# Performance work log

Measured on AMD Instinct MI355X. Metric: run time of the kernel, lower is better.

The kernel has to match this reference:

```python
import jax, jax.numpy as jnp
import numpy as np

D_MODEL = 1024
NUM_HEADS = 16
HEAD_DIM = D_MODEL // NUM_HEADS


def setup_inputs() -> dict:
    key = jax.random.key(0)
    ks = jax.random.split(key, 5)
    x = jax.random.normal(ks[0], (2, 2048, D_MODEL), dtype=jnp.float32)
    # torch nn.Linear init scale ~ U(-1/sqrt(in), 1/sqrt(in)); use small normals
    s = 1.0 / np.sqrt(D_MODEL)
    W_qkv = jax.random.normal(ks[1], (D_MODEL, 3 * D_MODEL), dtype=jnp.float32) * s
    b_qkv = jax.random.normal(ks[2], (3 * D_MODEL,), dtype=jnp.float32) * s
    W_out = jax.random.normal(ks[3], (D_MODEL, D_MODEL), dtype=jnp.float32) * s
    b_out = jax.random.normal(ks[4], (D_MODEL,), dtype=jnp.float32) * s
    return {"x": x, "W_qkv": W_qkv, "b_qkv": b_qkv, "W_out": W_out, "b_out": b_out}


def reference(x, W_qkv, b_qkv, W_out, b_out):
    B, S, _ = x.shape
    qkv = x @ W_qkv + b_qkv                                  # [B,S,3D]
    qkv = qkv.reshape(B, S, NUM_HEADS, 3 * HEAD_DIM).transpose(0, 2, 1, 3)  # [B,H,S,3d]
    q, k, v = jnp.split(qkv, 3, axis=-1)                     # each [B,H,S,d]
    scale = 1.0 / np.sqrt(HEAD_DIM)
    scores = jnp.einsum("bhqd,bhkd->bhqk", q, k) * scale      # [B,H,S,S]
    attn = jax.nn.softmax(scores, axis=-1)
    values = jnp.einsum("bhqk,bhkd->bhqd", attn, v)           # [B,H,S,d]
    values = values.transpose(0, 2, 1, 3).reshape(B, S, D_MODEL)
    return values @ W_out + b_out
```

## Files before the change

kernel.cpp:

```cpp
#include <hip/hip_runtime.h>


#define D_MODEL 1024
#define NHEAD   16
#define HDIM    64
#define SEQ     2048
#define BATCH   2
#define NTOK    (BATCH * SEQ)

typedef float    f32x4  __attribute__((ext_vector_type(4)));
typedef float    f32x16 __attribute__((ext_vector_type(16)));
typedef _Float16 f16x8  __attribute__((ext_vector_type(8)));
typedef _Float16 f16x4  __attribute__((ext_vector_type(4)));

#define GLOBAL_LOAD_LDS16(gptr, lptr)                                            \
    __builtin_amdgcn_global_load_lds(                                            \
        (const __attribute__((address_space(1))) unsigned int*)(gptr),           \
        (__attribute__((address_space(3))) unsigned int*)(lptr), 16, 0, 0)

__global__ __launch_bounds__(256) void prep_kernel(
    const float* __restrict__ x, _Float16* __restrict__ xh,
    const float* __restrict__ Wqkv, _Float16* __restrict__ wq_t,
    const float* __restrict__ Wout, _Float16* __restrict__ wo_t)
{
    const int bx = blockIdx.x;
    const int tid = threadIdx.x;
    if (bx < 4096) {
        const int i = (bx * 256 + tid) * 4;
        const float4 v = *(const float4*)&x[i];
        f16x4 hh;
        hh[0] = (_Float16)v.x; hh[1] = (_Float16)v.y;
        hh[2] = (_Float16)v.z; hh[3] = (_Float16)v.w;
        *(f16x4*)&xh[i] = hh;
        return;
    }
    __shared__ float ts[64][65];
    const float* W; _Float16* Wt; int N, n0, k0;
    if (bx < 4096 + 768) {
        const int local = bx - 4096;
        W = Wqkv; Wt = wq_t; N = 3072;
        n0 = (local % 48) * 64; k0 = (local / 48) * 64;
    } else {
        const int local = bx - 4864;
        W = Wout; Wt = wo_t; N = 1024;
        n0 = (local % 16) * 64; k0 = (local / 16) * 64;
    }
    {
        const int r = tid >> 2, c = (tid & 3) << 4;
        const float* src = W + (size_t)(k0 + r) * N + n0 + c;
        #pragma unroll
        for (int u = 0; u < 4; ++u)
            *(float4*)&ts[r][c + u * 4] = *(const float4*)&src[u * 4];
    }
    __syncthreads();
    {
        const int n = tid >> 2, kg = (tid & 3) << 4;
        f16x8 v0, v1;
        #pragma unroll
        for (int j = 0; j < 8; ++j) {
            v0[j] = (_Float16)ts[kg + j][n];
            v1[j] = (_Float16)ts[kg + 8 + j][n];
        }
        _Float16* dst = Wt + (size_t)(n0 + n) * D_MODEL + k0 + kg;
        *(f16x8*)&dst[0] = v0;
        *(f16x8*)&dst[8] = v1;
    }
}

__global__ __launch_bounds__(512) void gemm_qkv_kernel(
    const _Float16* __restrict__ A, const _Float16* __restrict__ Bt,
    const float* __restrict__ bias, _Float16* __restrict__ Cout,
    int M, int N, int K)
{
    __shared__ _Float16 lds[2][4096];
    const int tid = threadIdx.x;
    const int wave = tid >> 6, lane = tid & 63;
    const int quad = lane >> 4, l16 = lane & 15;
    const int m0 = blockIdx.y * 128, n0 = blockIdx.x * 128;
    const int wr = wave >> 1, wc = wave & 1;

    f32x4 acc[2][4] = {};

    const bool isA = wave < 4;
    const _Float16* gsrc = isA ? (A + (size_t)m0 * K) : (Bt + (size_t)n0 * K);
    _Float16* ldst = isA ? &lds[0][0] : &lds[1][0];
    const int sbase = (wave & 3) * 2;

    for (int k0 = 0; k0 < K; k0 += 32) {
        __syncthreads();
        #pragma unroll
        for (int j = 0; j < 2; ++j) {
            const int seg = sbase + j;
            const int chunk = seg >> 1;
            const int row = ((seg & 1) << 6) | lane;
            GLOBAL_LOAD_LDS16(gsrc + (size_t)row * K + k0 + chunk * 8, ldst + seg * 512);
        }
        __syncthreads();

        f16x8 a[2], b[4];
        #pragma unroll
        for (int mt = 0; mt < 2; ++mt)
            a[mt] = *(const f16x8*)&lds[0][quad * 1024 + (wr * 32 + mt * 16 + l16) * 8];
        #pragma unroll
        for (int nt = 0; nt < 4; ++nt)
            b[nt] = *(const f16x8*)&lds[1][quad * 1024 + (wc * 64 + nt * 16 + l16) * 8];
        #pragma unroll
        for (int mt = 0; mt < 2; ++mt)
            #pragma unroll
            for (int nt = 0; nt < 4; ++nt)
                acc[mt][nt] = __builtin_amdgcn_mfma_f32_16x16x32_f16(a[mt], b[nt], acc[mt][nt], 0, 0, 0);
    }

    #pragma unroll
    for (int nt = 0; nt < 4; ++nt) {
        const int col = n0 + wc * 64 + nt * 16 + l16;
        const float bv = bias[col];
        #pragma unroll
        for (int mt = 0; mt < 2; ++mt) {
            #pragma unroll
            for (int r = 0; r < 4; ++r) {
                const int row = m0 + wr * 32 + mt * 16 + quad * 4 + r;
                Cout[(size_t)row * N + col] = (_Float16)(acc[mt][nt][r] + bv);
            }
        }
    }
}

__global__ __launch_bounds__(512) void gemm_out_kernel(
    const _Float16* __restrict__ A, const _Float16* __restrict__ Bt,
    const float* __restrict__ bias, float* __restrict__ Cout)
{
    const int K = D_MODEL, N = D_MODEL;
    __shared__ _Float16 ldsA[4096];
    __shared__ _Float16 ldsB[2048];
    const int tid = threadIdx.x;
    const int wave = tid >> 6, lane = tid & 63;
    const int quad = lane >> 4, l16 = lane & 15;
    const int m0 = blockIdx.y * 128, n0 = blockIdx.x * 64;
    const int wr = wave >> 1, wc = wave & 1;

    f32x4 acc[2][2] = {};

    for (int k0 = 0; k0 < K; k0 += 32) {
        __syncthreads();
        if (wave < 4) {
            #pragma unroll
            for (int j = 0; j < 2; ++j) {
                const int seg = wave * 2 + j;
                const int chunk = seg >> 1;
                const int row = ((seg & 1) << 6) | lane;
                GLOBAL_LOAD_LDS16(A + (size_t)(m0 + row) * K + k0 + chunk * 8, ldsA + seg * 512);
            }
        } else {
            const int seg = wave - 4;
            GLOBAL_LOAD_LDS16(Bt + (size_t)(n0 + lane) * K + k0 + seg * 8, ldsB + seg * 512);
        }
        __syncthreads();

        f16x8 a[2], b[2];
        #pragma unroll
        for (int mt = 0; mt < 2; ++mt)
            a[mt] = *(const f16x8*)&ldsA[quad * 1024 + (wr * 32 + mt * 16 + l16) * 8];
        #pragma unroll
        for (int nt = 0; nt < 2; ++nt)
            b[nt] = *(const f16x8*)&ldsB[quad * 512 + (wc * 32 + nt * 16 + l16) * 8];
        #pragma unroll
        for (int mt = 0; mt < 2; ++mt)
            #pragma unroll
            for (int nt = 0; nt < 2; ++nt)
                acc[mt][nt] = __builtin_amdgcn_mfma_f32_16x16x32_f16(a[mt], b[nt], acc[mt][nt], 0, 0, 0);
    }

    #pragma unroll
    for (int nt = 0; nt < 2; ++nt) {
        const int col = n0 + wc * 32 + nt * 16 + l16;
        const float bv = bias[col];
        #pragma unroll
        for (int mt = 0; mt < 2; ++mt) {
            #pragma unroll
            for (int r = 0; r < 4; ++r) {
                const int row = m0 + wr * 32 + mt * 16 + quad * 4 + r;
                Cout[(size_t)row * N + col] = acc[mt][nt][r] + bv;
            }
        }
    }
}

__global__ __launch_bounds__(256) void swizzle_kv_kernel(
    const _Float16* __restrict__ qkv,
    _Float16* __restrict__ Ksw, _Float16* __restrict__ Vsw)
{
    __shared__ _Float16 ts[64][72];
    const int tid = threadIdx.x;
    const int s0 = blockIdx.x * 64, h = blockIdx.y, b = blockIdx.z;
    const size_t hsz = (size_t)8 * SEQ * 8;
    _Float16* kh = Ksw + (size_t)(b * NHEAD + h) * hsz;
    _Float16* vh = Vsw + (size_t)(b * NHEAD + h) * hsz;

    {
        const int s = s0 + (tid >> 2);
        const int dg = (tid & 3) << 4;
        const _Float16* src = qkv + (size_t)(b * SEQ + s) * (3 * D_MODEL) + h * (3 * HDIM) + HDIM + dg;
        const f16x8 v0 = *(const f16x8*)&src[0];
        const f16x8 v1 = *(const f16x8*)&src[8];
        const int c0 = dg >> 3;
        *(f16x8*)&kh[((size_t)c0 * SEQ + s) * 8]       = v0;
        *(f16x8*)&kh[((size_t)(c0 + 1) * SEQ + s) * 8] = v1;
    }
    {
        const int s = tid >> 2, dg = (tid & 3) << 4;
        const _Float16* src = qkv + (size_t)(b * SEQ + s0 + s) * (3 * D_MODEL) + h * (3 * HDIM) + 2 * HDIM + dg;
        *(f16x8*)&ts[s][dg]     = *(const f16x8*)&src[0];
        *(f16x8*)&ts[s][dg + 8] = *(const f16x8*)&src[8];
    }
    __syncthreads();
    {
        const int d = tid >> 2, sg = (tid & 3) << 4;
        f16x8 v0, v1;
        #pragma unroll
        for (int j = 0; j < 8; ++j) { v0[j] = ts[sg + j][d]; v1[j] = ts[sg + 8 + j][d]; }
        const int cs0 = (s0 + sg) >> 3;
        *(f16x8*)&vh[((size_t)cs0 * HDIM + d) * 8]       = v0;
        *(f16x8*)&vh[((size_t)(cs0 + 1) * HDIM + d) * 8] = v1;
    }
}

__global__ __launch_bounds__(256) void attn_mfma_kernel(
    const _Float16* __restrict__ qkv,
    const _Float16* __restrict__ Ksw, const _Float16* __restrict__ Vsw,
    _Float16* __restrict__ val)
{
    __shared__ _Float16 Ks[2][4096];
    __shared__ _Float16 Vts[2][4096];

    const int tid = threadIdx.x;
    const int wave = tid >> 6, lane = tid & 63;
    const int l31 = lane & 31, hi = lane >> 5;

    const int id = blockIdx.x;
    const int g  = (id & 7) * 64 + (id >> 3);
    const int qt = g & 15, hb = g >> 4;
    const int h  = hb & 15, b = hb >> 4;
    const int q0 = qt * 128;

    const size_t hsz = (size_t)8 * SEQ * 8;
    const _Float16* kh = Ksw + (size_t)(b * NHEAD + h) * hsz;
    const _Float16* vh = Vsw + (size_t)(b * NHEAD + h) * hsz;

    f16x8 qf[4];
    {
        const int row = q0 + wave * 32 + l31;
        const _Float16* src = qkv + (size_t)(b * SEQ + row) * (3 * D_MODEL) + h * (3 * HDIM) + hi * 8;
        #pragma unroll
        for (int kk = 0; kk < 4; ++kk) {
            const f16x8 t = *(const f16x8*)(src + kk * 16);
            #pragma unroll
            for (int j = 0; j < 8; ++j)
                qf[kk][j] = (_Float16)((float)t[j] * 0.1803368802f);
        }
    }

    f32x16 acc0 = {};
    f32x16 acc1 = {};
    float rs = 0.f;

    #pragma unroll
    for (int jj = 0; jj < 2; ++jj) {
        const int c = wave * 2 + jj;
        GLOBAL_LOAD_LDS16(kh + ((size_t)c * SEQ + lane) * 8, &Ks[0][c * 512]);
        GLOBAL_LOAD_LDS16(vh + ((size_t)c * HDIM + lane) * 8, &Vts[0][c * 512]);
    }
    __syncthreads();

    for (int kt = 0; kt < SEQ / 64; ++kt) {
        const int cur = kt & 1;

        if (kt + 1 < SEQ / 64) {
            #pragma unroll
            for (int jj = 0; jj < 2; ++jj) {
                const int c = wave * 2 + jj;
                GLOBAL_LOAD_LDS16(kh + ((size_t)c * SEQ + (kt + 1) * 64 + lane) * 8,
                                  &Ks[cur ^ 1][c * 512]);
                GLOBAL_LOAD_LDS16(vh + ((size_t)((kt + 1) * 8 + c) * HDIM + lane) * 8,
                                  &Vts[cur ^ 1][c * 512]);
            }
        }

        f32x16 s0 = {};
        f32x16 s1 = {};
        __builtin_amdgcn_s_setprio(1);
        #pragma unroll
        for (int kk = 0; kk < 4; ++kk) {
            const f16x8 k0 = *(const f16x8*)&Ks[cur][(kk * 2 + hi) * 512 + l31 * 8];
            const f16x8 k1 = *(const f16x8*)&Ks[cur][(kk * 2 + hi) * 512 + (32 + l31) * 8];
            s0 = __builtin_amdgcn_mfma_f32_32x32x16_f16(k0, qf[kk], s0, 0, 0, 0);
            s1 = __builtin_amdgcn_mfma_f32_32x32x16_f16(k1, qf[kk], s1, 0, 0, 0);
        }
        __builtin_amdgcn_s_setprio(0);

        f16x8 pa[4];
        #pragma unroll
        for (int half = 0; half < 2; ++half) {
            const f32x16 sv = half ? s1 : s0;
            float p[16];
            #pragma unroll
            for (int r = 0; r < 16; ++r)
                p[r] = __builtin_amdgcn_exp2f(sv[r]);
            #pragma unroll
            for (int r = 0; r < 16; r += 4)
                rs += (p[r] + p[r + 1]) + (p[r + 2] + p[r + 3]);

            union { f16x8 h; unsigned u[4]; } lo, hh;
            {
                const unsigned A = __builtin_bit_cast(unsigned, __builtin_amdgcn_cvt_pkrtz(p[0], p[1]));
                const unsigned B = __builtin_bit_cast(unsigned, __builtin_amdgcn_cvt_pkrtz(p[2], p[3]));
                const unsigned C = __builtin_bit_cast(unsigned, __builtin_amdgcn_cvt_pkrtz(p[4], p[5]));
                const unsigned D = __builtin_bit_cast(unsigned, __builtin_amdgcn_cvt_pkrtz(p[6], p[7]));
                const auto rac = __builtin_amdgcn_permlane32_swap(A, C, false, false);
                const auto rbd = __builtin_amdgcn_permlane32_swap(B, D, false, false);
                lo.u[0] = rac[0]; lo.u[1] = rbd[0]; lo.u[2] = rac[1]; lo.u[3] = rbd[1];
            }
            {
                const unsigned E = __builtin_bit_cast(unsigned, __builtin_amdgcn_cvt_pkrtz(p[8],  p[9]));
                const unsigned F = __builtin_bit_cast(unsigned, __builtin_amdgcn_cvt_pkrtz(p[10], p[11]));
                const unsigned G = __builtin_bit_cast(unsigned, __builtin_amdgcn_cvt_pkrtz(p[12], p[13]));
                const unsigned H = __builtin_bit_cast(unsigned, __builtin_amdgcn_cvt_pkrtz(p[14], p[15]));
                const auto reg = __builtin_amdgcn_permlane32_swap(E, G, false, false);
                const auto rfh = __builtin_amdgcn_permlane32_swap(F, H, false, false);
                hh.u[0] = reg[0]; hh.u[1] = rfh[0]; hh.u[2] = reg[1]; hh.u[3] = rfh[1];
            }
            pa[half * 2]     = lo.h;
            pa[half * 2 + 1] = hh.h;
        }

        __builtin_amdgcn_s_setprio(1);
        #pragma unroll
        for (int ks = 0; ks < 4; ++ks) {
            const f16x8 v0 = *(const f16x8*)&Vts[cur][(ks * 2 + hi) * 512 + l31 * 8];
            const f16x8 v1 = *(const f16x8*)&Vts[cur][(ks * 2 + hi) * 512 + (32 + l31) * 8];
            acc0 = __builtin_amdgcn_mfma_f32_32x32x16_f16(pa[ks], v0, acc0, 0, 0, 0);
            acc1 = __builtin_amdgcn_mfma_f32_32x32x16_f16(pa[ks], v1, acc1, 0, 0, 0);
        }
        __builtin_amdgcn_s_setprio(0);

        __syncthreads();
    }

    rs += __shfl_xor(rs, 32);
    const float inv = 1.f / rs;

    #pragma unroll
    for (int r = 0; r < 16; ++r) {
        const int qo = (r & 3) + 8 * (r >> 2) + 4 * hi;
        const float invr = __shfl(inv, qo);
        const int row = b * SEQ + q0 + wave * 32 + qo;
        val[(size_t)row * D_MODEL + h * HDIM + l31]      = (_Float16)(acc0[r] * invr);
        val[(size_t)row * D_MODEL + h * HDIM + 32 + l31] = (_Float16)(acc1[r] * invr);
    }
}

extern "C" void kernel_launch(void* const* d_in, const int* in_sizes, int n_in,
                              void* d_out, int out_size, void* d_ws, size_t ws_size,
                              hipStream_t stream)
{
    const float* x     = (const float*)d_in[0];
    const float* W_qkv = (const float*)d_in[1];
    const float* b_qkv = (const float*)d_in[2];
    const float* W_out = (const float*)d_in[3];
    const float* b_out = (const float*)d_in[4];

    char* ws = (char*)d_ws;
    _Float16* Ksw   = (_Float16*)ws;
    _Float16* val_h = (_Float16*)(ws + (8u << 20));
    _Float16* wq_t  = (_Float16*)(ws + (16u << 20));
    _Float16* wo_t  = (_Float16*)(ws + (22u << 20));
    _Float16* qkv_h = (_Float16*)(ws + (24u << 20));
    _Float16* x_h   = (_Float16*)(ws + (48u << 20));
    _Float16* Vsw   = (_Float16*)(ws + (48u << 20));

    prep_kernel<<<5120, 256, 0, stream>>>(x, x_h, W_qkv, wq_t, W_out, wo_t);
    gemm_qkv_kernel<<<dim3(3 * D_MODEL / 128, NTOK / 128), 512, 0, stream>>>(
        x_h, wq_t, b_qkv, qkv_h, NTOK, 3 * D_MODEL, D_MODEL);
    swizzle_kv_kernel<<<dim3(SEQ / 64, NHEAD, BATCH), 256, 0, stream>>>(qkv_h, Ksw, Vsw);
    attn_mfma_kernel<<<dim3(512, 1, 1), 256, 0, stream>>>(qkv_h, Ksw, Vsw, val_h);
    gemm_out_kernel<<<dim3(D_MODEL / 64, NTOK / 128), 512, 0, stream>>>(
        val_h, wo_t, b_out, (float*)d_out);
}
```

Measured before the change: 223.7 us.

## Process two 32-row query tiles per wave to reuse K/V fragments and interleave softmax

Each wave now handles 64 query rows (two 32-row sub-tiles), so a block covers 256 queries and the grid halves to 256 blocks. K and V fragments are loaded from LDS into registers once per iteration and shared by both sub-tiles, halving LDS reads and global K/V traffic per query. The QK MFMAs of the second sub-tile are issued before the first sub-tile's softmax so that exp work can overlap matrix ops, and the explicit setprio hints are dropped. The cost is much higher register pressure and only 256 blocks, which may underfill the 256 CUs and reduce latency hiding.

Measured after the change: 228.4 us. 1.02x slower.

```diff
diff --git a/kernel.cpp b/kernel.cpp
--- a/kernel.cpp
+++ b/kernel.cpp
@@ -225,6 +225,44 @@
     }
 }
 
+__device__ __forceinline__ void softmax_frag(
+    const f32x16 s0, const f32x16 s1, float& rs, f16x8 pa[4])
+{
+    #pragma unroll
+    for (int half = 0; half < 2; ++half) {
+        const f32x16 sv = half ? s1 : s0;
+        float p[16];
+        #pragma unroll
+        for (int r = 0; r < 16; ++r)
+            p[r] = __builtin_amdgcn_exp2f(sv[r]);
+        #pragma unroll
+        for (int r = 0; r < 16; r += 4)
+            rs += (p[r] + p[r + 1]) + (p[r + 2] + p[r + 3]);
+
+        union { f16x8 hv; unsigned u[4]; } lo, hh;
+        {
+            const unsigned A = __builtin_bit_cast(unsigned, __builtin_amdgcn_cvt_pkrtz(p[0], p[1]));
+            const unsigned B = __builtin_bit_cast(unsigned, __builtin_amdgcn_cvt_pkrtz(p[2], p[3]));
+            const unsigned C = __builtin_bit_cast(unsigned, __builtin_amdgcn_cvt_pkrtz(p[4], p[5]));
+            const unsigned D = __builtin_bit_cast(unsigned, __builtin_amdgcn_cvt_pkrtz(p[6], p[7]));
+            const auto rac = __builtin_amdgcn_permlane32_swap(A, C, false, false);
+            const auto rbd = __builtin_amdgcn_permlane32_swap(B, D, false, false);
+            lo.u[0] = rac[0]; lo.u[1] = rbd[0]; lo.u[2] = rac[1]; lo.u[3] = rbd[1];
+        }
+        {
+            const unsigned E = __builtin_bit_cast(unsigned, __builtin_amdgcn_cvt_pkrtz(p[8],  p[9]));
+            const unsigned F = __builtin_bit_cast(unsigned, __builtin_amdgcn_cvt_pkrtz(p[10], p[11]));
+            const unsigned G = __builtin_bit_cast(unsigned, __builtin_amdgcn_cvt_pkrtz(p[12], p[13]));
+            const unsigned H = __builtin_bit_cast(unsigned, __builtin_amdgcn_cvt_pkrtz(p[14], p[15]));
+            const auto reg = __builtin_amdgcn_permlane32_swap(E, G, false, false);
+            const auto rfh = __builtin_amdgcn_permlane32_swap(F, H, false, false);
+            hh.u[0] = reg[0]; hh.u[1] = rfh[0]; hh.u[2] = reg[1]; hh.u[3] = rfh[1];
+        }
+        pa[half * 2]     = lo.hv;
+        pa[half * 2 + 1] = hh.hv;
+    }
+}
+
 __global__ __launch_bounds__(256) void attn_mfma_kernel(
     const _Float16* __restrict__ qkv,
     const _Float16* __restrict__ Ksw, const _Float16* __restrict__ Vsw,
@@ -238,31 +276,35 @@
     const int l31 = lane & 31, hi = lane >> 5;
 
     const int id = blockIdx.x;
-    const int g  = (id & 7) * 64 + (id >> 3);
-    const int qt = g & 15, hb = g >> 4;
+    const int g  = (id & 7) * 32 + (id >> 3);
+    const int qt = g & 7, hb = g >> 3;
     const int h  = hb & 15, b = hb >> 4;
-    const int q0 = qt * 128;
+    const int q0 = qt * 256;
 
     const size_t hsz = (size_t)8 * SEQ * 8;
     const _Float16* kh = Ksw + (size_t)(b * NHEAD + h) * hsz;
     const _Float16* vh = Vsw + (size_t)(b * NHEAD + h) * hsz;
 
-    f16x8 qf[4];
-    {
-        const int row = q0 + wave * 32 + l31;
-        const _Float16* src = qkv + (size_t)(b * SEQ + row) * (3 * D_MODEL) + h * (3 * HDIM) + hi * 8;
+    f16x8 qfa[4], qfb[4];
+    {
+        const int rowa = q0 + wave * 64 + l31;
+        const _Float16* srca = qkv + (size_t)(b * SEQ + rowa) * (3 * D_MODEL) + h * (3 * HDIM) + hi * 8;
+        const _Float16* srcb = srca + (size_t)32 * (3 * D_MODEL);
         #pragma unroll
         for (int kk = 0; kk < 4; ++kk) {
-            const f16x8 t = *(const f16x8*)(src + kk * 16);
-            #pragma unroll
-            for (int j = 0; j < 8; ++j)
-                qf[kk][j] = (_Float16)((float)t[j] * 0.1803368802f);
-        }
-    }
-
-    f32x16 acc0 = {};
-    f32x16 acc1 = {};
-    float rs = 0.f;
+            const f16x8 ta = *(const f16x8*)(srca + kk * 16);
+            const f16x8 tb = *(const f16x8*)(srcb + kk * 16);
+            #pragma unroll
+            for (int j = 0; j < 8; ++j) {
+                qfa[kk][j] = (_Float16)((float)ta[j] * 0.1803368802f);
+                qfb[kk][j] = (_Float16)((float)tb[j] * 0.1803368802f);
+            }
+        }
+    }
+
+    f32x16 acca0 = {}, acca1 = {};
+    f32x16 accb0 = {}, accb1 = {};
+    float rsa = 0.f, rsb = 0.f;
 
     #pragma unroll
     for (int jj = 0; jj < 2; ++jj) {
@@ -286,76 +328,69 @@
             }
         }
 
-        f32x16 s0 = {};
-        f32x16 s1 = {};
-        __builtin_amdgcn_s_setprio(1);
+        f16x8 kf0[4], kf1[4];
         #pragma unroll
         for (int kk = 0; kk < 4; ++kk) {
-            const f16x8 k0 = *(const f16x8*)&Ks[cur][(kk * 2 + hi) * 512 + l31 * 8];
-            const f16x8 k1 = *(const f16x8*)&Ks[cur][(kk * 2 + hi) * 512 + (32 + l31) * 8];
-            s0 = __builtin_amdgcn_mfma_f32_32x32x16_f16(k0, qf[kk], s0, 0, 0, 0);
-            s1 = __builtin_amdgcn_mfma_f32_32x32x16_f16(k1, qf[kk], s1, 0, 0, 0);
-        }
-        __builtin_amdgcn_s_setprio(0);
-
-        f16x8 pa[4];
-        #pragma unroll
-        for (int half = 0; half < 2; ++half) {
-            const f32x16 sv = half ? s1 : s0;
-            float p[16];
-            #pragma unroll
-            for (int r = 0; r < 16; ++r)
-                p[r] = __builtin_amdgcn_exp2f(sv[r]);
-            #pragma unroll
-            for (int r = 0; r < 16; r += 4)
-                rs += (p[r] + p[r + 1]) + (p[r + 2] + p[r + 3]);
-
-            union { f16x8 h; unsigned u[4]; } lo, hh;
-            {
-                const unsigned A = __builtin_bit_cast(unsigned, __builtin_amdgcn_cvt_pkrtz(p[0], p[1]));
-                const unsigned B = __builtin_bit_cast(unsigned, __builtin_amdgcn_cvt_pkrtz(p[2], p[3]));
-                const unsigned C = __builtin_bit_cast(unsigned, __builtin_amdgcn_cvt_pkrtz(p[4], p[5]));
-                const unsigned D = __builtin_bit_cast(unsigned, __builtin_amdgcn_cvt_pkrtz(p[6], p[7]));
-                const auto rac = __builtin_amdgcn_permlane32_swap(A, C, false, false);
-                const auto rbd = __builtin_amdgcn_permlane32_swap(B, D, false, false);
-                lo.u[0] = rac[0]; lo.u[1] = rbd[0]; lo.u[2] = rac[1]; lo.u[3] = rbd[1];
-            }
-            {
-                const unsigned E = __builtin_bit_cast(unsigned, __builtin_amdgcn_cvt_pkrtz(p[8],  p[9]));
-                const unsigned F = __builtin_bit_cast(unsigned, __builtin_amdgcn_cvt_pkrtz(p[10], p[11]));
-                const unsigned G = __builtin_bit_cast(unsigned, __builtin_amdgcn_cvt_pkrtz(p[12], p[13]));
-                const unsigned H = __builtin_bit_cast(unsigned, __builtin_amdgcn_cvt_pkrtz(p[14], p[15]));
-                const auto reg = __builtin_amdgcn_permlane32_swap(E, G, false, false);
-                const auto rfh = __builtin_amdgcn_permlane32_swap(F, H, false, false);
-                hh.u[0] = reg[0]; hh.u[1] = rfh[0]; hh.u[2] = reg[1]; hh.u[3] = rfh[1];
-            }
-            pa[half * 2]     = lo.h;
-            pa[half * 2 + 1] = hh.h;
-        }
-
-        __builtin_amdgcn_s_setprio(1);
+            kf0[kk] = *(const f16x8*)&Ks[cur][(kk * 2 + hi) * 512 + l31 * 8];
+            kf1[kk] = *(const f16x8*)&Ks[cur][(kk * 2 + hi) * 512 + (32 + l31) * 8];
+        }
+
+        f32x16 sa0 = {}, sa1 = {};
+        #pragma unroll
+        for (int kk = 0; kk < 4; ++kk) {
+            sa0 = __builtin_amdgcn_mfma_f32_32x32x16_f16(kf0[kk], qfa[kk], sa0, 0, 0, 0);
+            sa1 = __builtin_amdgcn_mfma_f32_32x32x16_f16(kf1[kk], qfa[kk], sa1, 0, 0, 0);
+        }
+
+        f16x8 vf0[4], vf1[4];
         #pragma unroll
         for (int ks = 0; ks < 4; ++ks) {
-            const f16x8 v0 = *(const f16x8*)&Vts[cur][(ks * 2 + hi) * 512 + l31 * 8];
-            const f16x8 v1 = *(const f16x8*)&Vts[cur][(ks * 2 + hi) * 512 + (32 + l31) * 8];
-            acc0 = __builtin_amdgcn_mfma_f32_32x32x16_f16(pa[ks], v0, acc0, 0, 0, 0);
-            acc1 = __builtin_amdgcn_mfma_f32_32x32x16_f16(pa[ks], v1, acc1, 0, 0, 0);
-        }
-        __builtin_amdgcn_s_setprio(0);
+            vf0[ks] = *(const f16x8*)&Vts[cur][(ks * 2 + hi) * 512 + l31 * 8];
+            vf1[ks] = *(const f16x8*)&Vts[cur][(ks * 2 + hi) * 512 + (32 + l31) * 8];
+        }
+
+        f32x16 sb0 = {}, sb1 = {};
+        #pragma unroll
+        for (int kk = 0; kk < 4; ++kk) {
+            sb0 = __builtin_amdgcn_mfma_f32_32x32x16_f16(kf0[kk], qfb[kk], sb0, 0, 0, 0);
+            sb1 = __builtin_amdgcn_mfma_f32_32x32x16_f16(kf1[kk], qfb[kk], sb1, 0, 0, 0);
+        }
+
+        f16x8 paa[4];
+        softmax_frag(sa0, sa1, rsa, paa);
+        #pragma unroll
+        for (int ks = 0; ks < 4; ++ks) {
+            acca0 = __builtin_amdgcn_mfma_f32_32x32x16_f16(paa[ks], vf0[ks], acca0, 0, 0, 0);
+            acca1 = __builtin_amdgcn_mfma_f32_32x32x16_f16(paa[ks], vf1[ks], acca1, 0, 0, 0);
+        }
+
+        f16x8 pab[4];
+        softmax_frag(sb0, sb1, rsb, pab);
+        #pragma unroll
+        for (int ks = 0; ks < 4; ++ks) {
+            accb0 = __builtin_amdgcn_mfma_f32_32x32x16_f16(pab[ks], vf0[ks], accb0, 0, 0, 0);
+            accb1 = __builtin_amdgcn_mfma_f32_32x32x16_f16(pab[ks], vf1[ks], accb1, 0, 0, 0);
+        }
 
         __syncthreads();
     }
 
-    rs += __shfl_xor(rs, 32);
-    const float inv = 1.f / rs;
+    rsa += __shfl_xor(rsa, 32);
+    rsb += __shfl_xor(rsb, 32);
+    const float inva = 1.f / rsa;
+    const float invb = 1.f / rsb;
 
     #pragma unroll
     for (int r = 0; r < 16; ++r) {
         const int qo = (r & 3) + 8 * (r >> 2) + 4 * hi;
-        const float invr = __shfl(inv, qo);
-        const int row = b * SEQ + q0 + wave * 32 + qo;
-        val[(size_t)row * D_MODEL + h * HDIM + l31]      = (_Float16)(acc0[r] * invr);
-        val[(size_t)row * D_MODEL + h * HDIM + 32 + l31] = (_Float16)(acc1[r] * invr);
+        const float ia = __shfl(inva, qo);
+        const float ib = __shfl(invb, qo);
+        const int rowa = b * SEQ + q0 + wave * 64 + qo;
+        const int rowb = rowa + 32;
+        val[(size_t)rowa * D_MODEL + h * HDIM + l31]      = (_Float16)(acca0[r] * ia);
+        val[(size_t)rowa * D_MODEL + h * HDIM + 32 + l31] = (_Float16)(acca1[r] * ia);
+        val[(size_t)rowb * D_MODEL + h * HDIM + l31]      = (_Float16)(accb0[r] * ib);
+        val[(size_t)rowb * D_MODEL + h * HDIM + 32 + l31] = (_Float16)(accb1[r] * ib);
     }
 }
 
@@ -382,7 +417,7 @@
     gemm_qkv_kernel<<<dim3(3 * D_MODEL / 128, NTOK / 128), 512, 0, stream>>>(
         x_h, wq_t, b_qkv, qkv_h, NTOK, 3 * D_MODEL, D_MODEL);
     swizzle_kv_kernel<<<dim3(SEQ / 64, NHEAD, BATCH), 256, 0, stream>>>(qkv_h, Ksw, Vsw);
-    attn_mfma_kernel<<<dim3(512, 1, 1), 256, 0, stream>>>(qkv_h, Ksw, Vsw, val_h);
+    attn_mfma_kernel<<<dim3(256, 1, 1), 256, 0, stream>>>(qkv_h, Ksw, Vsw, val_h);
     gemm_out_kernel<<<dim3(D_MODEL / 64, NTOK / 128), 512, 0, stream>>>(
         val_h, wo_t, b_out, (float*)d_out);
 }
```

## Enlarge attention blocks to 8 waves with 256-query tiles and 128-key stages

Applied to the files above, without the earlier changes.

The attention kernel now runs 512 threads per block, each block covering 256 queries, so there are half as many blocks (256). Each loop iteration stages 128 keys instead of 64, split into two 64-key sub-tiles, which halves the number of barriers and doubles the reuse of each staged K/V tile across waves. The cost is fewer blocks than before (256 on a chip with about as many CUs, so possible load imbalance), more LDS per block (64KB), and larger barrier groups. The softmax code is moved into a helper function.

Result: faster. 216.6 us (-3.2%).

```diff
diff --git a/kernel.cpp b/kernel.cpp
--- a/kernel.cpp
+++ b/kernel.cpp
@@ -225,23 +225,61 @@
     }
 }
 
-__global__ __launch_bounds__(256) void attn_mfma_kernel(
+__device__ __forceinline__ void softmax_frag(
+    const f32x16 s0, const f32x16 s1, float& rs, f16x8 pa[4])
+{
+    #pragma unroll
+    for (int half = 0; half < 2; ++half) {
+        const f32x16 sv = half ? s1 : s0;
+        float p[16];
+        #pragma unroll
+        for (int r = 0; r < 16; ++r)
+            p[r] = __builtin_amdgcn_exp2f(sv[r]);
+        #pragma unroll
+        for (int r = 0; r < 16; r += 4)
+            rs += (p[r] + p[r + 1]) + (p[r + 2] + p[r + 3]);
+
+        union { f16x8 hv; unsigned u[4]; } lo, hh;
+        {
+            const unsigned A = __builtin_bit_cast(unsigned, __builtin_amdgcn_cvt_pkrtz(p[0], p[1]));
+            const unsigned B = __builtin_bit_cast(unsigned, __builtin_amdgcn_cvt_pkrtz(p[2], p[3]));
+            const unsigned C = __builtin_bit_cast(unsigned, __builtin_amdgcn_cvt_pkrtz(p[4], p[5]));
+            const unsigned D = __builtin_bit_cast(unsigned, __builtin_amdgcn_cvt_pkrtz(p[6], p[7]));
+            const auto rac = __builtin_amdgcn_permlane32_swap(A, C, false, false);
+            const auto rbd = __builtin_amdgcn_permlane32_swap(B, D, false, false);
+            lo.u[0] = rac[0]; lo.u[1] = rbd[0]; lo.u[2] = rac[1]; lo.u[3] = rbd[1];
+        }
+        {
+            const unsigned E = __builtin_bit_cast(unsigned, __builtin_amdgcn_cvt_pkrtz(p[8],  p[9]));
+            const unsigned F = __builtin_bit_cast(unsigned, __builtin_amdgcn_cvt_pkrtz(p[10], p[11]));
+            const unsigned G = __builtin_bit_cast(unsigned, __builtin_amdgcn_cvt_pkrtz(p[12], p[13]));
+            const unsigned H = __builtin_bit_cast(unsigned, __builtin_amdgcn_cvt_pkrtz(p[14], p[15]));
+            const auto reg = __builtin_amdgcn_permlane32_swap(E, G, false, false);
+            const auto rfh = __builtin_amdgcn_permlane32_swap(F, H, false, false);
+            hh.u[0] = reg[0]; hh.u[1] = rfh[0]; hh.u[2] = reg[1]; hh.u[3] = rfh[1];
+        }
+        pa[half * 2]     = lo.hv;
+        pa[half * 2 + 1] = hh.hv;
+    }
+}
+
+__global__ __launch_bounds__(512) void attn_mfma_kernel(
     const _Float16* __restrict__ qkv,
     const _Float16* __restrict__ Ksw, const _Float16* __restrict__ Vsw,
     _Float16* __restrict__ val)
 {
-    __shared__ _Float16 Ks[2][4096];
-    __shared__ _Float16 Vts[2][4096];
+    __shared__ _Float16 Ks[2][8192];
+    __shared__ _Float16 Vts[2][8192];
 
     const int tid = threadIdx.x;
     const int wave = tid >> 6, lane = tid & 63;
     const int l31 = lane & 31, hi = lane >> 5;
 
     const int id = blockIdx.x;
-    const int g  = (id & 7) * 64 + (id >> 3);
-    const int qt = g & 15, hb = g >> 4;
+    const int g  = (id & 7) * 32 + (id >> 3);
+    const int qt = g & 7, hb = g >> 3;
     const int h  = hb & 15, b = hb >> 4;
-    const int q0 = qt * 128;
+    const int q0 = qt * 256;
 
     const size_t hsz = (size_t)8 * SEQ * 8;
     const _Float16* kh = Ksw + (size_t)(b * NHEAD + h) * hsz;
@@ -264,84 +302,60 @@
     f32x16 acc1 = {};
     float rs = 0.f;
 
+    const int sidx0 = wave * 2;
     #pragma unroll
-    for (int jj = 0; jj < 2; ++jj) {
-        const int c = wave * 2 + jj;
-        GLOBAL_LOAD_LDS16(kh + ((size_t)c * SEQ + lane) * 8, &Ks[0][c * 512]);
-        GLOBAL_LOAD_LDS16(vh + ((size_t)c * HDIM + lane) * 8, &Vts[0][c * 512]);
+    for (int j = 0; j < 2; ++j) {
+        const int idx = sidx0 + j;
+        const int u = idx >> 3, c = idx & 7;
+        GLOBAL_LOAD_LDS16(kh + ((size_t)c * SEQ + u * 64 + lane) * 8, &Ks[0][idx * 512]);
+        GLOBAL_LOAD_LDS16(vh + ((size_t)(u * 8 + c) * HDIM + lane) * 8, &Vts[0][idx * 512]);
     }
     __syncthreads();
 
-    for (int kt = 0; kt < SEQ / 64; ++kt) {
+    for (int kt = 0; kt < SEQ / 128; ++kt) {
         const int cur = kt & 1;
 
-        if (kt + 1 < SEQ / 64) {
-            #pragma unroll
-            for (int jj = 0; jj < 2; ++jj) {
-                const int c = wave * 2 + jj;
-                GLOBAL_LOAD_LDS16(kh + ((size_t)c * SEQ + (kt + 1) * 64 + lane) * 8,
-                                  &Ks[cur ^ 1][c * 512]);
-                GLOBAL_LOAD_LDS16(vh + ((size_t)((kt + 1) * 8 + c) * HDIM + lane) * 8,
-                                  &Vts[cur ^ 1][c * 512]);
-            }
-        }
-
-        f32x16 s0 = {};
-        f32x16 s1 = {};
-        __builtin_amdgcn_s_setprio(1);
-        #pragma unroll
-        for (int kk = 0; kk < 4; ++kk) {
-            const f16x8 k0 = *(const f16x8*)&Ks[cur][(kk * 2 + hi) * 512 + l31 * 8];
-            const f16x8 k1 = *(const f16x8*)&Ks[cur][(kk * 2 + hi) * 512 + (32 + l31) * 8];
-            s0 = __builtin_amdgcn_mfma_f32_32x32x16_f16(k0, qf[kk], s0, 0, 0, 0);
-            s1 = __builtin_amdgcn_mfma_f32_32x32x16_f16(k1, qf[kk], s1, 0, 0, 0);
-        }
-        __builtin_amdgcn_s_setprio(0);
-
-        f16x8 pa[4];
-        #pragma unroll
-        for (int half = 0; half < 2; ++half) {
-            const f32x16 sv = half ? s1 : s0;
-            float p[16];
-            #pragma unroll
-            for (int r = 0; r < 16; ++r)
-                p[r] = __builtin_amdgcn_exp2f(sv[r]);
-            #pragma unroll
-            for (int r = 0; r < 16; r += 4)
-                rs += (p[r] + p[r + 1]) + (p[r + 2] + p[r + 3]);
-
-            union { f16x8 h; unsigned u[4]; } lo, hh;
-            {
-                const unsigned A = __builtin_bit_cast(unsigned, __builtin_amdgcn_cvt_pkrtz(p[0], p[1]));
-                const unsigned B = __builtin_bit_cast(unsigned, __builtin_amdgcn_cvt_pkrtz(p[2], p[3]));
-                const unsigned C = __builtin_bit_cast(unsigned, __builtin_amdgcn_cvt_pkrtz(p[4], p[5]));
-                const unsigned D = __builtin_bit_cast(unsigned, __builtin_amdgcn_cvt_pkrtz(p[6], p[7]));
-                const auto rac = __builtin_amdgcn_permlane32_swap(A, C, false, false);
-                const auto rbd = __builtin_amdgcn_permlane32_swap(B, D, false, false);
-                lo.u[0] = rac[0]; lo.u[1] = rbd[0]; lo.u[2] = rac[1]; lo.u[3] = rbd[1];
-            }
-            {
-                const unsigned E = __builtin_bit_cast(unsigned, __builtin_amdgcn_cvt_pkrtz(p[8],  p[9]));
-                const unsigned F = __builtin_bit_cast(unsigned, __builtin_amdgcn_cvt_pkrtz(p[10], p[11]));
-                const unsigned G = __builtin_bit_cast(unsigned, __builtin_amdgcn_cvt_pkrtz(p[12], p[13]));
-                const unsigned H = __builtin_bit_cast(unsigned, __builtin_amdgcn_cvt_pkrtz(p[14], p[15]));
-                const auto reg = __builtin_amdgcn_permlane32_swap(E, G, false, false);
-                const auto rfh = __builtin_amdgcn_permlane32_swap(F, H, false, false);
-                hh.u[0] = reg[0]; hh.u[1] = rfh[0]; hh.u[2] = reg[1]; hh.u[3] = rfh[1];
-            }
-            pa[half * 2]     = lo.h;
-            pa[half * 2 + 1] = hh.h;
-        }
-
-        __builtin_amdgcn_s_setprio(1);
-        #pragma unroll
-        for (int ks = 0; ks < 4; ++ks) {
-            const f16x8 v0 = *(const f16x8*)&Vts[cur][(ks * 2 + hi) * 512 + l31 * 8];
-            const f16x8 v1 = *(const f16x8*)&Vts[cur][(ks * 2 + hi) * 512 + (32 + l31) * 8];
-            acc0 = __builtin_amdgcn_mfma_f32_32x32x16_f16(pa[ks], v0, acc0, 0, 0, 0);
-            acc1 = __builtin_amdgcn_mfma_f32_32x32x16_f16(pa[ks], v1, acc1, 0, 0, 0);
-        }
-        __builtin_amdgcn_s_setprio(0);
+        if (kt + 1 < SEQ / 128) {
+            #pragma unroll
+            for (int j = 0; j < 2; ++j) {
+                const int idx = sidx0 + j;
+                const int u = idx >> 3, c = idx & 7;
+                GLOBAL_LOAD_LDS16(kh + ((size_t)c * SEQ + (kt + 1) * 128 + u * 64 + lane) * 8,
+                                  &Ks[cur ^ 1][idx * 512]);
+                GLOBAL_LOAD_LDS16(vh + ((size_t)((kt + 1) * 16 + u * 8 + c) * HDIM + lane) * 8,
+                                  &Vts[cur ^ 1][idx * 512]);
+            }
+        }
+
+        #pragma unroll
+        for (int u = 0; u < 2; ++u) {
+            const _Float16* ksub = &Ks[cur][u * 4096];
+            const _Float16* vsub = &Vts[cur][u * 4096];
+
+            f32x16 s0 = {}, s1 = {};
+            __builtin_amdgcn_s_setprio(1);
+            #pragma unroll
+            for (int kk = 0; kk < 4; ++kk) {
+                const f16x8 k0 = *(const f16x8*)&ksub[(kk * 2 + hi) * 512 + l31 * 8];
+                const f16x8 k1 = *(const f16x8*)&ksub[(kk * 2 + hi) * 512 + (32 + l31) * 8];
+                s0 = __builtin_amdgcn_mfma_f32_32x32x16_f16(k0, qf[kk], s0, 0, 0, 0);
+                s1 = __builtin_amdgcn_mfma_f32_32x32x16_f16(k1, qf[kk], s1, 0, 0, 0);
+            }
+            __builtin_amdgcn_s_setprio(0);
+
+            f16x8 pa[4];
+            softmax_frag(s0, s1, rs, pa);
+
+            __builtin_amdgcn_s_setprio(1);
+            #pragma unroll
+            for (int ks = 0; ks < 4; ++ks) {
+                const f16x8 v0 = *(const f16x8*)&vsub[(ks * 2 + hi) * 512 + l31 * 8];
+                const f16x8 v1 = *(const f16x8*)&vsub[(ks * 2 + hi) * 512 + (32 + l31) * 8];
+                acc0 = __builtin_amdgcn_mfma_f32_32x32x16_f16(pa[ks], v0, acc0, 0, 0, 0);
+                acc1 = __builtin_amdgcn_mfma_f32_32x32x16_f16(pa[ks], v1, acc1, 0, 0, 0);
+            }
+            __builtin_amdgcn_s_setprio(0);
+        }
 
         __syncthreads();
     }
@@ -382,7 +396,7 @@
     gemm_qkv_kernel<<<dim3(3 * D_MODEL / 128, NTOK / 128), 512, 0, stream>>>(
         x_h, wq_t, b_qkv, qkv_h, NTOK, 3 * D_MODEL, D_MODEL);
     swizzle_kv_kernel<<<dim3(SEQ / 64, NHEAD, BATCH), 256, 0, stream>>>(qkv_h, Ksw, Vsw);
-    attn_mfma_kernel<<<dim3(512, 1, 1), 256, 0, stream>>>(qkv_h, Ksw, Vsw, val_h);
+    attn_mfma_kernel<<<dim3(256, 1, 1), 512, 0, stream>>>(qkv_h, Ksw, Vsw, val_h);
     gemm_out_kernel<<<dim3(D_MODEL / 64, NTOK / 128), 512, 0, stream>>>(
         val_h, wo_t, b_out, (float*)d_out);
 }
```
